# Kernel optimization log

Hardware: AMD Instinct MI355X
Metric: run time of the kernel (lower is better)

Reference implementation:

```python
import jax, jax.numpy as jnp
import numpy as np

N_E = 8192      # codebook size
E_DIM = 256     # codebook dim
BETA = 0.25

def setup_inputs() -> dict:
    key = jax.random.key(0)
    k1, k2 = jax.random.split(key)
    z = jax.random.normal(k1, (4, E_DIM, 16, 16, 16), dtype=jnp.float32)
    weight = jax.random.normal(k2, (N_E, E_DIM), dtype=jnp.float32)
    return {"z": z, "weight": weight}

def reference(z, weight):
    # b c d h w -> b d h w c
    z_t = jnp.transpose(z, (0, 2, 3, 4, 1))
    zf = z_t.reshape(-1, E_DIM)                          # [N, e_dim]
    # l2 pairwise distances: |z|^2 + |w|^2 - 2 z.w^T
    d = (jnp.sum(zf * zf, axis=1, keepdims=True)
         + jnp.sum(weight * weight, axis=1)
         - 2.0 * jnp.einsum('bd,nd->bn', zf, weight))    # [N, n_e]
    idx = jnp.argmin(d, axis=1)                          # [N]
    z_q = weight[idx].reshape(z_t.shape)                 # gather lookup
    # perplexity from cluster assignment histogram (avoids dense one-hot)
    counts = jax.ops.segment_sum(jnp.ones_like(idx, dtype=z.dtype), idx,
                                 num_segments=N_E)
    avg_probs = counts / zf.shape[0]
    perplexity = jnp.exp(-jnp.sum(avg_probs * jnp.log(avg_probs + 1e-10)))
    # commitment loss (z_q detached)
    loss = BETA * jnp.mean((jax.lax.stop_gradient(z_q) - z_t) ** 2)
    # straight-through estimator
    z_q_st = z_t + jax.lax.stop_gradient(z_q - z_t)
    out = jnp.transpose(z_q_st, (0, 4, 1, 2, 3))         # b d h w c -> b c d h w
    return out, loss, perplexity, idx
```

## Files before the change

kernel.cpp:

```cpp
#include <hip/hip_runtime.h>
#include <stdint.h>


#define M_TOTAL 16384
#define N_CODES 8192
#define KDIM    256
#define SPATIAL 4096
#define NSPLIT  8
#define CODES_PER_SPLIT  1024
#define CHUNK_CODES      16
#define CHUNKS_PER_SPLIT 64
#define CHUNK_BYTES      9216
#define CHUNK_HALFS      4608
#define M_BLOCK          128

typedef _Float16 v8hf __attribute__((ext_vector_type(8)));
typedef _Float16 v4hf __attribute__((ext_vector_type(4)));
typedef float    v4f  __attribute__((ext_vector_type(4)));

#define WAITCNT_VM3   0x0F73
#define WAITCNT_VM0   0x0F70

__global__ __launch_bounds__(256) void prep_kernel(
    const float* __restrict__ w, const float* __restrict__ z,
    _Float16* __restrict__ wpk, _Float16* __restrict__ z_pk,
    int* __restrict__ counts, double* __restrict__ loss_acc)
{
    const int t = threadIdx.x;
    const int lane = t & 63;
    if (blockIdx.x < 2048) {
        const int n = blockIdx.x * 4 + (t >> 6);
        v4f v = ((const v4f*)(w + (size_t)n * KDIM))[lane];
        v4hf hv;
        float s = 0.0f;
#pragma unroll
        for (int j = 0; j < 4; j++) {
            float f = v[j];
            s += f * f;
            hv[j] = (_Float16)f;
        }
        const int chunk = n >> 4;
        const int row   = n & 15;
        const int ks = lane >> 3;
        const int qq = (lane >> 1) & 3;
        const int hh = lane & 1;
        size_t off = (size_t)chunk * CHUNK_HALFS + ks * 512 + qq * 128 + row * 8 + hh * 4;
        *(v4hf*)(wpk + off) = hv;
#pragma unroll
        for (int o = 32; o >= 1; o >>= 1) s += __shfl_xor(s, o);
        if (lane == 0) {
            float* hwp = (float*)((char*)wpk + (size_t)chunk * CHUNK_BYTES + 8192);
            hwp[row] = 1024.0f - 0.5f * s;
        }
        const int gi = blockIdx.x * 256 + t;
        if (gi < N_CODES) counts[gi] = 0;
        if (gi == 0) *loss_acc = 0.0;
    } else {
        __shared__ float lt[32][KDIM + 4];
        const int zi = blockIdx.x - 2048;
        const int i0 = zi * 32;
        const int b  = i0 >> 12;
        const int s0 = i0 & (SPATIAL - 1);
        for (int e = t; e < 32 * KDIM; e += 256) {
            const int c = e >> 5, rr = e & 31;
            lt[rr][c] = z[((size_t)b << 20) + ((size_t)c << 12) + s0 + rr];
        }
        __syncthreads();
#pragma unroll
        for (int j = 0; j < 4; j++) {
            const int o  = t + j * 256;
            const int g  = o >> 9;
            const int ks = (o >> 6) & 7;
            const int q  = (o >> 4) & 3;
            const int r  = o & 15;
            const int row = g * 16 + r;
            const int k0  = ks * 32 + q * 8;
            v8hf hv;
#pragma unroll
            for (int u = 0; u < 8; u++) hv[u] = (_Float16)lt[row][k0 + u];
            const int grp = (i0 >> 4) + g;
            *(v8hf*)(z_pk + (size_t)grp * 4096 + ks * 512 + q * 128 + r * 8) = hv;
        }
    }
}

__device__ __forceinline__ void top2max_merge(uint32_t& v1, int& i1, uint32_t& v2, int& i2,
                                              uint32_t o1, int oi1, uint32_t o2, int oi2) {
    bool ob = (o1 > v1) || (o1 == v1 && oi1 < i1);
    uint32_t n1v, n2v; int n1i, n2i;
    if (ob) {
        bool t2 = (v1 > o2) || (v1 == o2 && i1 < oi2);
        n1v = o1; n1i = oi1;
        n2v = t2 ? v1 : o2; n2i = t2 ? i1 : oi2;
    } else {
        bool t2 = (o1 > v2) || (o1 == v2 && oi1 < i2);
        n1v = v1; n1i = i1;
        n2v = t2 ? o1 : v2; n2i = t2 ? oi1 : i2;
    }
    v1 = n1v; i1 = n1i; v2 = n2v; i2 = n2i;
}

__global__ __launch_bounds__(256, 4) void gemm_kernel(
    const _Float16* __restrict__ z_pk,
    const _Float16* __restrict__ wpk,
    int4* __restrict__ candbuf)
{
    __shared__ __align__(16) _Float16 lds[3][CHUNK_HALFS];

    const int bid   = blockIdx.x;
    const int split = bid & 7;
    const int rb    = bid >> 3;
    const int i0    = rb * M_BLOCK;
    const int tid   = threadIdx.x;
    const int wid   = tid >> 6;
    const int lane  = tid & 63;
    const int r     = lane & 15;
    const int q     = lane >> 4;

    const char* wsplit = (const char*)wpk + (size_t)split * CHUNKS_PER_SPLIT * CHUNK_BYTES;

    auto stage = [&](int c, _Float16* lbh) {
        const char* gb = wsplit + (size_t)c * CHUNK_BYTES;
        char* lb = (char*)lbh;
#pragma unroll
        for (int j = 0; j < 2; j++) {
            const int o = (wid * 2 + j) * 1024 + lane * 16;
            __builtin_amdgcn_global_load_lds(
                (const __attribute__((address_space(1))) void*)(gb + o),
                (__attribute__((address_space(3))) void*)(lb + o), 16, 0, 0);
        }
        const int oh = 8192 + wid * 256 + lane * 4;
        __builtin_amdgcn_global_load_lds(
            (const __attribute__((address_space(1))) void*)(gb + oh),
            (__attribute__((address_space(3))) void*)(lb + oh), 4, 0, 0);
    };

    stage(0, lds[0]);
    stage(1, lds[1]);

    v8hf a[2][8];
    {
        const int g0 = rb * 8 + wid * 2;
#pragma unroll
        for (int mt = 0; mt < 2; mt++)
#pragma unroll
        for (int ks = 0; ks < 8; ks++)
            a[mt][ks] = *(const v8hf*)(z_pk + (size_t)(g0 + mt) * 4096 + ks * 512 + q * 128 + r * 8);
    }

    uint32_t k1[2][4], k2[2][4];
#pragma unroll
    for (int mt = 0; mt < 2; mt++)
#pragma unroll
    for (int g = 0; g < 4; g++) { k1[mt][g] = 0u; k2[mt][g] = 0u; }

    auto compute = [&](int it, const _Float16* lbh) {
        const char* lb = (const char*)lbh;
        const float hwv = *(const float*)(lb + 8192 + r * 4);
        v4f acc[2];
#pragma unroll
        for (int mt = 0; mt < 2; mt++) acc[mt] = (v4f){hwv, hwv, hwv, hwv};

        __builtin_amdgcn_s_setprio(1);
#pragma unroll
        for (int ks = 0; ks < 8; ks++) {
            v8hf bh = *(const v8hf*)(lb + ks * 1024 + lane * 16);
#pragma unroll
            for (int mt = 0; mt < 2; mt++)
                acc[mt] = __builtin_amdgcn_mfma_f32_16x16x32_f16(a[mt][ks], bh, acc[mt], 0, 0, 0);
        }
        __builtin_amdgcn_s_setprio(0);

        const uint32_t tag = (uint32_t)it;
#pragma unroll
        for (int mt = 0; mt < 2; mt++)
#pragma unroll
        for (int g = 0; g < 4; g++) {
            uint32_t key = (__float_as_uint(acc[mt][g]) & 0xFFFFFFC0u) | tag;
            uint32_t o1 = k1[mt][g];
            uint32_t k2n;
            asm("v_med3_u32 %0, %1, %2, %3" : "=v"(k2n) : "v"(key), "v"(o1), "v"(k2[mt][g]));
            k2[mt][g] = k2n;
            k1[mt][g] = key > o1 ? key : o1;
        }
    };

    const _Float16 *pA = lds[0], *pB = lds[1];
    _Float16 *pC = lds[2];
#pragma unroll 1
    for (int it = 0; it < CHUNKS_PER_SPLIT - 2; it++) {
        __builtin_amdgcn_s_waitcnt(WAITCNT_VM3);
        __builtin_amdgcn_s_barrier();
        __builtin_amdgcn_sched_barrier(0);
        compute(it, pA);
        stage(it + 2, pC);
        const _Float16* tmp = pA; pA = pB; pB = pC; pC = (_Float16*)tmp;
    }
    __builtin_amdgcn_s_waitcnt(WAITCNT_VM3);
    __builtin_amdgcn_s_barrier();
    __builtin_amdgcn_sched_barrier(0);
    compute(CHUNKS_PER_SPLIT - 2, pA);
    __builtin_amdgcn_s_waitcnt(WAITCNT_VM0);
    __builtin_amdgcn_s_barrier();
    __builtin_amdgcn_sched_barrier(0);
    compute(CHUNKS_PER_SPLIT - 1, pB);

    const int nsbase = split * CODES_PER_SPLIT + r;
#pragma unroll
    for (int mt = 0; mt < 2; mt++) {
#pragma unroll
        for (int g = 0; g < 4; g++) {
            uint32_t K1 = k1[mt][g], K2 = k2[mt][g];
            int n1 = nsbase + (int)((K1 & 63u) << 4);
            int n2 = nsbase + (int)((K2 & 63u) << 4);
#pragma unroll
            for (int off = 1; off < 16; off <<= 1) {
                uint32_t o1 = __shfl_xor(K1, off);
                int     on1 = __shfl_xor(n1, off);
                uint32_t o2 = __shfl_xor(K2, off);
                int     on2 = __shfl_xor(n2, off);
                top2max_merge(K1, n1, K2, n2, o1, on1, o2, on2);
            }
            if (r == 0) {
                const int row = i0 + wid * 32 + mt * 16 + q * 4 + g;
                candbuf[(size_t)row * NSPLIT + split] = make_int4((int)K1, n1, (int)K2, n2);
            }
        }
    }
}

__global__ __launch_bounds__(256) void finish_kernel(
    const float* __restrict__ z, const float* __restrict__ weight,
    const int4* __restrict__ candbuf,
    int* __restrict__ counts, double* __restrict__ loss_acc,
    float* __restrict__ out, float* __restrict__ out_idx_f)
{
    __shared__ int4  s_cand[32][NSPLIT];
    __shared__ float s_zw[32][KDIM + 1];
    __shared__ int   s_fi[32];
    __shared__ double s_loss[4];

    const int i0 = blockIdx.x * 32;
    const int b  = i0 >> 12;
    const int s0 = i0 & (SPATIAL - 1);
    const int t  = threadIdx.x;

    s_cand[t >> 3][t & 7] = candbuf[(size_t)(i0 + (t >> 3)) * NSPLIT + (t & 7)];

    for (int e = t; e < 32 * KDIM; e += 256) {
        const int c = e >> 5, rr = e & 31;
        s_zw[rr][c] = z[((size_t)b << 20) + ((size_t)c << 12) + s0 + rr];
    }
    __syncthreads();

    const int row = t >> 3, seg = t & 7;
    float zs[32];
#pragma unroll
    for (int j = 0; j < 32; j++) zs[j] = s_zw[row][seg * 32 + j];

    float da[2 * NSPLIT];
    float dmin_a = 3.4e38f;
#pragma unroll
    for (int sp = 0; sp < NSPLIT; sp++) {
        int4 c = s_cand[row][sp];
        da[sp * 2]     = 2048.0f - 2.0f * __uint_as_float((uint32_t)c.x & 0xFFFFFFC0u);
        da[sp * 2 + 1] = 2048.0f - 2.0f * __uint_as_float((uint32_t)c.z & 0xFFFFFFC0u);
        dmin_a = fminf(dmin_a, fminf(da[sp * 2], da[sp * 2 + 1]));
    }
    const float cutoff = dmin_a + 0.5f;

    double dbest = 1e300; int nbest = 0x7fffffff;
#pragma unroll 1
    for (int c = 0; c < 2 * NSPLIT; c++) {
        if (da[c] > cutoff) continue;
        int4 cc = s_cand[row][c >> 1];
        const int n = (c & 1) ? cc.w : cc.y;
        const v4f* wr = (const v4f*)(weight + (size_t)n * KDIM + seg * 32);
        double d = 0.0;
#pragma unroll
        for (int jj = 0; jj < 8; jj++) {
            v4f wv = wr[jj];
#pragma unroll
            for (int u = 0; u < 4; u++) {
                double df = (double)zs[jj * 4 + u] - (double)wv[u];
                d += df * df;
            }
        }
#pragma unroll
        for (int o = 1; o < 8; o <<= 1) d += __shfl_xor(d, o);
        if (d < dbest || (d == dbest && n < nbest)) { dbest = d; nbest = n; }
    }

    double lsum = 0.0;
    if (seg == 0) {
        s_fi[row] = nbest;
        out_idx_f[i0 + row] = (float)nbest;
        atomicAdd(&counts[nbest], 1);
        lsum = dbest;
    }
#pragma unroll
    for (int o = 1; o < 64; o <<= 1) lsum += __shfl_xor(lsum, o);
    if ((t & 63) == 0) s_loss[t >> 6] = lsum;
    __syncthreads();
    if (t == 0) atomicAdd(loss_acc, s_loss[0] + s_loss[1] + s_loss[2] + s_loss[3]);

    for (int e = t; e < 32 * KDIM; e += 256) {
        const int rr = e >> 8, c = e & 255;
        s_zw[rr][c] = weight[(size_t)s_fi[rr] * KDIM + c];
    }
    __syncthreads();
    const int m = t & 31, c0 = t >> 5;
    const size_t obase = ((size_t)b << 20) + (size_t)(s0 + m);
    for (int c = c0; c < KDIM; c += 8)
        out[obase + ((size_t)c << 12)] = s_zw[m][c];
}

__global__ void finalize_kernel(const int* __restrict__ counts,
                                const double* __restrict__ loss_acc,
                                float* __restrict__ out_scalars)
{
    const int t = threadIdx.x;
    double s = 0.0;
    for (int n = t; n < N_CODES; n += 256) {
        double p = (double)counts[n] / (double)M_TOTAL;
        s -= p * log(p + 1e-10);
    }
#pragma unroll
    for (int o = 32; o >= 1; o >>= 1) s += __shfl_xor(s, o);
    __shared__ double sds[4];
    if ((t & 63) == 0) sds[t >> 6] = s;
    __syncthreads();
    if (t == 0) {
        double tot = sds[0] + sds[1] + sds[2] + sds[3];
        out_scalars[0] = (float)(0.25 * (*loss_acc) / (double)(M_TOTAL * KDIM));
        out_scalars[1] = (float)exp(tot);
    }
}

extern "C" void kernel_launch(void* const* d_in, const int* in_sizes, int n_in,
                              void* d_out, int out_size, void* d_ws, size_t ws_size,
                              hipStream_t stream) {
    const float* z      = (const float*)d_in[0];
    const float* weight = (const float*)d_in[1];
    float* out = (float*)d_out;

    size_t off = 0;
    auto carve = [&](size_t bytes) {
        void* p = (char*)d_ws + off;
        off += (bytes + 255) & ~(size_t)255;
        return p;
    };
    _Float16* wpk     = (_Float16*)carve((size_t)(N_CODES / CHUNK_CODES) * CHUNK_BYTES);
    _Float16* z_pk    = (_Float16*)carve((size_t)M_TOTAL * KDIM * 2);
    int4*     candbuf = (int4*)    carve((size_t)M_TOTAL * NSPLIT * 16);
    int*      counts  = (int*)     carve((size_t)N_CODES * 4);
    double*   lossac  = (double*)  carve(16);

    float* out_scalars = out + (size_t)4 * KDIM * SPATIAL;
    float* out_idx_f   = out_scalars + 2;

    prep_kernel<<<dim3(2560), dim3(256), 0, stream>>>(weight, z, wpk, z_pk, counts, lossac);
    gemm_kernel<<<dim3(M_TOTAL / M_BLOCK * NSPLIT), dim3(256), 0, stream>>>(z_pk, wpk, candbuf);
    finish_kernel<<<dim3(M_TOTAL / 32), dim3(256), 0, stream>>>(
        z, weight, candbuf, counts, lossac, out, out_idx_f);
    finalize_kernel<<<dim3(1), dim3(256), 0, stream>>>(counts, lossac, out_scalars);
}
```

Before: 186.8 us.

## Fuse finalize into finish via last-block counter and vectorize z transposes

Removes the separate single-block finalize launch: the last finish block to increment an atomic counter computes the perplexity and loss scalars. It also replaces the scalar strided z loads in prep and finish, and the output stores in finish, with 4-wide vector accesses, changing the shared-memory padding to suit. This saves one kernel launch and raises memory transaction width, at the cost of a global atomic handshake and more shared-memory bank conflicts in the transposed writes.

```diff
diff --git a/kernel.cpp b/kernel.cpp
--- a/kernel.cpp
+++ b/kernel.cpp
@@ -24,7 +24,8 @@
 __global__ __launch_bounds__(256) void prep_kernel(
     const float* __restrict__ w, const float* __restrict__ z,
     _Float16* __restrict__ wpk, _Float16* __restrict__ z_pk,
-    int* __restrict__ counts, double* __restrict__ loss_acc)
+    int* __restrict__ counts, double* __restrict__ loss_acc,
+    unsigned int* __restrict__ done)
 {
     const int t = threadIdx.x;
     const int lane = t & 63;
@@ -55,15 +56,19 @@
         const int gi = blockIdx.x * 256 + t;
         if (gi < N_CODES) counts[gi] = 0;
         if (gi == 0) *loss_acc = 0.0;
+        if (gi == 1) *done = 0u;
     } else {
-        __shared__ float lt[32][KDIM + 4];
+        __shared__ float lt[32][KDIM + 5];
         const int zi = blockIdx.x - 2048;
         const int i0 = zi * 32;
         const int b  = i0 >> 12;
         const int s0 = i0 & (SPATIAL - 1);
-        for (int e = t; e < 32 * KDIM; e += 256) {
-            const int c = e >> 5, rr = e & 31;
-            lt[rr][c] = z[((size_t)b << 20) + ((size_t)c << 12) + s0 + rr];
+        for (int e = t; e < 32 * KDIM / 4; e += 256) {
+            const int c  = e >> 3;
+            const int r4 = (e & 7) * 4;
+            const v4f v = *(const v4f*)(z + ((size_t)b << 20) + ((size_t)c << 12) + s0 + r4);
+#pragma unroll
+            for (int j = 0; j < 4; j++) lt[r4 + j][c] = v[j];
         }
         __syncthreads();
 #pragma unroll
@@ -233,12 +238,15 @@
     const float* __restrict__ z, const float* __restrict__ weight,
     const int4* __restrict__ candbuf,
     int* __restrict__ counts, double* __restrict__ loss_acc,
-    float* __restrict__ out, float* __restrict__ out_idx_f)
+    unsigned int* __restrict__ done,
+    float* __restrict__ out, float* __restrict__ out_scalars,
+    float* __restrict__ out_idx_f)
 {
     __shared__ int4  s_cand[32][NSPLIT];
     __shared__ float s_zw[32][KDIM + 1];
     __shared__ int   s_fi[32];
     __shared__ double s_loss[4];
+    __shared__ int   s_last;
 
     const int i0 = blockIdx.x * 32;
     const int b  = i0 >> 12;
@@ -247,9 +255,12 @@
 
     s_cand[t >> 3][t & 7] = candbuf[(size_t)(i0 + (t >> 3)) * NSPLIT + (t & 7)];
 
-    for (int e = t; e < 32 * KDIM; e += 256) {
-        const int c = e >> 5, rr = e & 31;
-        s_zw[rr][c] = z[((size_t)b << 20) + ((size_t)c << 12) + s0 + rr];
+    for (int e = t; e < 32 * KDIM / 4; e += 256) {
+        const int c  = e >> 3;
+        const int r4 = (e & 7) * 4;
+        const v4f v = *(const v4f*)(z + ((size_t)b << 20) + ((size_t)c << 12) + s0 + r4);
+#pragma unroll
+        for (int j = 0; j < 4; j++) s_zw[r4 + j][c] = v[j];
     }
     __syncthreads();
 
@@ -309,30 +320,42 @@
         s_zw[rr][c] = weight[(size_t)s_fi[rr] * KDIM + c];
     }
     __syncthreads();
-    const int m = t & 31, c0 = t >> 5;
-    const size_t obase = ((size_t)b << 20) + (size_t)(s0 + m);
-    for (int c = c0; c < KDIM; c += 8)
-        out[obase + ((size_t)c << 12)] = s_zw[m][c];
-}
-
-__global__ void finalize_kernel(const int* __restrict__ counts,
-                                const double* __restrict__ loss_acc,
-                                float* __restrict__ out_scalars)
-{
-    const int t = threadIdx.x;
+
+    {
+        const int m4 = (t & 7) * 4, cc0 = t >> 3;
+        const size_t ob = ((size_t)b << 20) + (size_t)(s0 + m4);
+        for (int c = cc0; c < KDIM; c += 32) {
+            v4f v;
+#pragma unroll
+            for (int j = 0; j < 4; j++) v[j] = s_zw[m4 + j][c];
+            *(v4f*)(out + ob + ((size_t)c << 12)) = v;
+        }
+    }
+
+    __syncthreads();
+    if (t == 0) {
+        __threadfence();
+        s_last = (atomicAdd(done, 1u) == (unsigned)(M_TOTAL / 32) - 1u);
+    }
+    __syncthreads();
+    if (!s_last) return;
+
     double s = 0.0;
     for (int n = t; n < N_CODES; n += 256) {
-        double p = (double)counts[n] / (double)M_TOTAL;
-        s -= p * log(p + 1e-10);
+        const int c = __hip_atomic_load(&counts[n], __ATOMIC_RELAXED, __HIP_MEMORY_SCOPE_AGENT);
+        if (c) {
+            const double p = (double)c / (double)M_TOTAL;
+            s -= p * log(p + 1e-10);
+        }
     }
 #pragma unroll
     for (int o = 32; o >= 1; o >>= 1) s += __shfl_xor(s, o);
-    __shared__ double sds[4];
-    if ((t & 63) == 0) sds[t >> 6] = s;
+    if ((t & 63) == 0) s_loss[t >> 6] = s;
     __syncthreads();
     if (t == 0) {
-        double tot = sds[0] + sds[1] + sds[2] + sds[3];
-        out_scalars[0] = (float)(0.25 * (*loss_acc) / (double)(M_TOTAL * KDIM));
+        const double tot = s_loss[0] + s_loss[1] + s_loss[2] + s_loss[3];
+        const double l = __hip_atomic_load(loss_acc, __ATOMIC_RELAXED, __HIP_MEMORY_SCOPE_AGENT);
+        out_scalars[0] = (float)(0.25 * l / (double)(M_TOTAL * KDIM));
         out_scalars[1] = (float)exp(tot);
     }
 }
@@ -355,13 +378,13 @@
     int4*     candbuf = (int4*)    carve((size_t)M_TOTAL * NSPLIT * 16);
     int*      counts  = (int*)     carve((size_t)N_CODES * 4);
     double*   lossac  = (double*)  carve(16);
+    unsigned int* done= (unsigned int*)carve(256);
 
     float* out_scalars = out + (size_t)4 * KDIM * SPATIAL;
     float* out_idx_f   = out_scalars + 2;
 
-    prep_kernel<<<dim3(2560), dim3(256), 0, stream>>>(weight, z, wpk, z_pk, counts, lossac);
+    prep_kernel<<<dim3(2560), dim3(256), 0, stream>>>(weight, z, wpk, z_pk, counts, lossac, done);
     gemm_kernel<<<dim3(M_TOTAL / M_BLOCK * NSPLIT), dim3(256), 0, stream>>>(z_pk, wpk, candbuf);
     finish_kernel<<<dim3(M_TOTAL / 32), dim3(256), 0, stream>>>(
-        z, weight, candbuf, counts, lossac, out, out_idx_f);
-    finalize_kernel<<<dim3(1), dim3(256), 0, stream>>>(counts, lossac, out_scalars);
-}
+        z, weight, candbuf, counts, lossac, done, out, out_scalars, out_idx_f);
+}
```

New measurement: 200.2 us. +7.1%, slower.
